# Optimization experiments

Measured on AMD Instinct MI355X. Metric: run time of the kernel, lower is better.

The kernel has to match this reference:

```python
import jax, jax.numpy as jnp
import numpy as np

B, T, F, D = 4, 512, 512, 256


def setup_inputs() -> dict:
    key = jax.random.key(0)
    ks = jax.random.split(key, 7)
    x = jax.random.normal(ks[0], (B, T, F), jnp.float32)
    state = jnp.zeros((B, D, D), jnp.float32)
    init = lambda k, shape, fan: jax.random.normal(k, shape, jnp.float32) / np.sqrt(fan).astype(np.float32)
    Wk = init(ks[1], (F, D), F)
    Wq = init(ks[2], (F, D), F)
    Wv = init(ks[3], (F, D), F)
    Wbeta = init(ks[4], (F, 1), F)
    gamma = jnp.ones((F,), jnp.float32)
    beta_ln = jnp.zeros((F,), jnp.float32)
    Wsc = init(ks[5], (F, D), F)
    bsc = jnp.zeros((D,), jnp.float32)
    return dict(x=x, state=state, Wk=Wk, Wq=Wq, Wv=Wv, Wbeta=Wbeta,
                gamma=gamma, beta_ln=beta_ln, Wsc=Wsc, bsc=bsc)


def _layernorm(x, gamma, beta):
    mu = x.mean(-1, keepdims=True)
    var = x.var(-1, keepdims=True)  # ddof=0, matches torch LayerNorm
    return (x - mu) * jax.lax.rsqrt(var + 1e-5) * gamma + beta


def reference(x, state, Wk, Wq, Wv, Wbeta, gamma, beta_ln, Wsc, bsc):
    xn = _layernorm(x, gamma, beta_ln)                       # [B,T,F]
    K = jax.nn.relu(xn @ Wk)                                 # [B,T,D]
    Q = jax.nn.relu(xn @ Wq)                                 # [B,T,D]
    V = xn @ Wv                                              # [B,T,D]
    beta = jax.nn.sigmoid(xn @ Wbeta)                        # [B,T,1]
    # sum normalization
    K = K / (1e-5 + K.sum(-1, keepdims=True))
    Q = Q / (1e-5 + Q.sum(-1, keepdims=True))

    def step(s, inp):
        k, v, b = inp                                        # k,v:[B,D], b:[B,1]
        vbar = jnp.einsum('bij,bj->bi', s, k)                # retrieve
        s = s + (b * (v - vbar))[:, :, None] * k[:, None, :] # outer-product write
        return s, s

    Kt = jnp.moveaxis(K, 1, 0)  # [T,B,D]
    Vt = jnp.moveaxis(V, 1, 0)
    bt = jnp.moveaxis(beta, 1, 0)  # [T,B,1]
    _, states = jax.lax.scan(step, state, (Kt, Vt, bt))      # [T,B,D,D]
    states = jnp.moveaxis(states, 0, 1)                      # [B,T,D,D]

    y = jnp.einsum('btij,btj->bti', states, Q)               # [B,T,D]
    y = y + xn @ Wsc + bsc                                   # residual shortcut
    return y, states
```

## Files before the change

kernel.cpp:

```cpp
#include <hip/hip_runtime.h>
#include <math.h>

#define Bc 4
#define Tc 512
#define Fc 512
#define Dc 256
#define RPB 8
#define PF 4
#define CH 16
#define RS 4
#define NC (Tc / CH)

typedef float floatx4 __attribute__((ext_vector_type(4)));

__device__ __forceinline__ float wred(float v) {
#pragma unroll
  for (int off = 32; off; off >>= 1) v += __shfl_xor(v, off, 64);
  return v;
}

__device__ __forceinline__ float rl(float v, int l) {
  return __int_as_float(__builtin_amdgcn_readlane(__float_as_int(v), l));
}

__device__ __forceinline__ void wred2_dpp(float& a, float& c) {
#define DPP_STEP(ctrl, rmask)                                                 \
  {                                                                           \
    float ta = __int_as_float(__builtin_amdgcn_update_dpp(                    \
        0, __float_as_int(a), (ctrl), (rmask), 0xf, true));                   \
    float tc = __int_as_float(__builtin_amdgcn_update_dpp(                    \
        0, __float_as_int(c), (ctrl), (rmask), 0xf, true));                   \
    a += ta;                                                                  \
    c += tc;                                                                  \
  }
  DPP_STEP(0x111, 0xf)
  DPP_STEP(0x112, 0xf)
  DPP_STEP(0x114, 0xf)
  DPP_STEP(0x118, 0xf)
  DPP_STEP(0x142, 0xa)
  DPP_STEP(0x143, 0xc)
#undef DPP_STEP
  a = rl(a, 63);
  c = rl(c, 63);
}

__global__ __launch_bounds__(256) void proj_kernel(
    const float* __restrict__ x, const float* __restrict__ Wk,
    const float* __restrict__ Wq, const float* __restrict__ Wv,
    const float* __restrict__ Wb, const float* __restrict__ gamma,
    const float* __restrict__ beta_ln, const float* __restrict__ Wsc,
    const float* __restrict__ bsc, float* __restrict__ Ko,
    float* __restrict__ Qo, float* __restrict__ Vo, float* __restrict__ ysco,
    float* __restrict__ betao, float* __restrict__ kqo) {
  __shared__ __align__(16) float xn[RPB][Fc];
  __shared__ float red[4][32];
  __shared__ float fin[32];

  const int tid = threadIdx.x;
  const int wave = tid >> 6, lane = tid & 63;
  const int row0 = blockIdx.x * RPB;

#pragma unroll
  for (int rr = 0; rr < 2; ++rr) {
    const int r = wave * 2 + rr;
    const float* xr = x + (size_t)(row0 + r) * Fc;
    float4 a = *(const float4*)&xr[lane * 8];
    float4 b = *(const float4*)&xr[lane * 8 + 4];
    float s8 = a.x + a.y + a.z + a.w + b.x + b.y + b.z + b.w;
    float mu = wred(s8) * (1.0f / Fc);
    float d0 = a.x - mu, d1 = a.y - mu, d2 = a.z - mu, d3 = a.w - mu;
    float d4 = b.x - mu, d5 = b.y - mu, d6 = b.z - mu, d7 = b.w - mu;
    float sq = d0 * d0 + d1 * d1 + d2 * d2 + d3 * d3 + d4 * d4 + d5 * d5 +
               d6 * d6 + d7 * d7;
    float var = wred(sq) * (1.0f / Fc);
    float rs = rsqrtf(var + 1e-5f);
    float4 g0 = *(const float4*)&gamma[lane * 8];
    float4 g1 = *(const float4*)&gamma[lane * 8 + 4];
    float4 bl0 = *(const float4*)&beta_ln[lane * 8];
    float4 bl1 = *(const float4*)&beta_ln[lane * 8 + 4];
    float4 o0 = make_float4(d0 * rs * g0.x + bl0.x, d1 * rs * g0.y + bl0.y,
                            d2 * rs * g0.z + bl0.z, d3 * rs * g0.w + bl0.w);
    float4 o1 = make_float4(d4 * rs * g1.x + bl1.x, d5 * rs * g1.y + bl1.y,
                            d6 * rs * g1.z + bl1.z, d7 * rs * g1.w + bl1.w);
    *(float4*)&xn[r][lane * 8] = o0;
    *(float4*)&xn[r][lane * 8 + 4] = o1;
  }
  __syncthreads();

  const int d = tid;
  float accK[RPB], accQ[RPB], accV[RPB], accS[RPB];
#pragma unroll
  for (int r = 0; r < RPB; ++r) accK[r] = accQ[r] = accV[r] = accS[r] = 0.0f;

  for (int f = 0; f < Fc; f += 4) {
    float wk[4], wq[4], wv[4], ws[4];
#pragma unroll
    for (int ff = 0; ff < 4; ++ff) {
      wk[ff] = Wk[(size_t)(f + ff) * Dc + d];
      wq[ff] = Wq[(size_t)(f + ff) * Dc + d];
      wv[ff] = Wv[(size_t)(f + ff) * Dc + d];
      ws[ff] = Wsc[(size_t)(f + ff) * Dc + d];
    }
#pragma unroll
    for (int r = 0; r < RPB; ++r) {
      float4 xr = *(const float4*)&xn[r][f];
      accK[r] = fmaf(xr.w, wk[3], fmaf(xr.z, wk[2], fmaf(xr.y, wk[1], fmaf(xr.x, wk[0], accK[r]))));
      accQ[r] = fmaf(xr.w, wq[3], fmaf(xr.z, wq[2], fmaf(xr.y, wq[1], fmaf(xr.x, wq[0], accQ[r]))));
      accV[r] = fmaf(xr.w, wv[3], fmaf(xr.z, wv[2], fmaf(xr.y, wv[1], fmaf(xr.x, wv[0], accV[r]))));
      accS[r] = fmaf(xr.w, ws[3], fmaf(xr.z, ws[2], fmaf(xr.y, ws[1], fmaf(xr.x, ws[0], accS[r]))));
    }
  }

  float pk[RPB], pq[RPB];
#pragma unroll
  for (int r = 0; r < RPB; ++r) {
    pk[r] = fmaxf(accK[r], 0.0f);
    pq[r] = fmaxf(accQ[r], 0.0f);
  }
#pragma unroll
  for (int r = 0; r < RPB; ++r) {
    float p0 = wred(pk[r]);
    float p1 = wred(pq[r]);
    float p2 = wred(pk[r] * pq[r]);
    float pb = xn[r][tid] * Wb[tid] + xn[r][tid + 256] * Wb[tid + 256];
    float p3 = wred(pb);
    if (lane == 0) {
      red[wave][r * 4 + 0] = p0;
      red[wave][r * 4 + 1] = p1;
      red[wave][r * 4 + 2] = p2;
      red[wave][r * 4 + 3] = p3;
    }
  }
  __syncthreads();
  if (tid < 32) fin[tid] = red[0][tid] + red[1][tid] + red[2][tid] + red[3][tid];
  __syncthreads();

#pragma unroll
  for (int r = 0; r < RPB; ++r) {
    size_t row = (size_t)(row0 + r);
    float invK = 1.0f / (1e-5f + fin[r * 4 + 0]);
    float invQ = 1.0f / (1e-5f + fin[r * 4 + 1]);
    Ko[row * Dc + d] = pk[r] * invK;
    Qo[row * Dc + d] = pq[r] * invQ;
    Vo[row * Dc + d] = accV[r];
    ysco[row * Dc + d] = accS[r] + bsc[d];
  }
  if (tid < RPB) {
    size_t row = (size_t)(row0 + tid);
    float invK = 1.0f / (1e-5f + fin[tid * 4 + 0]);
    float invQ = 1.0f / (1e-5f + fin[tid * 4 + 1]);
    betao[row] = 1.0f / (1.0f + expf(-fin[tid * 4 + 3]));
    kqo[row] = fin[tid * 4 + 2] * invK * invQ;
  }
}

__global__ __launch_bounds__(512) void scan_kernel(
    const float* __restrict__ S0, const float* __restrict__ K,
    const float* __restrict__ Q, const float* __restrict__ V,
    const float* __restrict__ ysc, const float* __restrict__ beta,
    const float* __restrict__ kq, float* __restrict__ yout,
    float* __restrict__ states) {
  __shared__ __align__(16) float ring_k[RS][CH][Dc];
  __shared__ float2 ring_uy[RS][CH][4];
  __shared__ int prog_a[4];
  __shared__ int prog_b[4];

  const int tid = threadIdx.x;
  const int wave = tid >> 6, lane = tid & 63;
  const int bid = blockIdx.x;
  const int xcd = bid & 7;
  const int slot = bid >> 3;
  const int b = xcd >> 1;
  const int sub = ((xcd & 1) << 5) | slot;
  const int i0 = sub * 4;

  if (tid < 4) {
    prog_a[tid] = 0;
    prog_b[tid] = 0;
  }
  __syncthreads();

  if (wave < 4) {
    const int i = i0 + wave;
    float4 s = *(const float4*)&S0[((size_t)(b * Dc + i)) * Dc + lane * 4];

    const float* Kb = K + (size_t)b * Tc * Dc;
    const float* Qb = Q + (size_t)b * Tc * Dc;
    const float* Vb = V + (size_t)b * Tc * Dc;
    const float* Yb = ysc + (size_t)b * Tc * Dc;
    const float* bb_p = beta + (size_t)b * Tc;
    const float* kq_p = kq + (size_t)b * Tc;

    float4 kb[PF], qb[PF];
#pragma unroll
    for (int j = 0; j < PF; ++j) {
      kb[j] = *(const float4*)&Kb[(size_t)j * Dc + lane * 4];
      qb[j] = *(const float4*)&Qb[(size_t)j * Dc + lane * 4];
    }
    const int sl = lane & 15;
    float vcur = Vb[(size_t)sl * Dc + i];
    float ycur = Yb[(size_t)sl * Dc + i];
    float bcur = bb_p[sl];
    float kqcur = kq_p[sl];

    for (int c = 0; c < NC; ++c) {
      if (c >= RS) {
        const int need = c - RS + 1;
#pragma unroll
        for (int m = 0; m < 4; ++m) {
          while (__hip_atomic_load(&prog_b[m], __ATOMIC_ACQUIRE,
                                   __HIP_MEMORY_SCOPE_WORKGROUP) < need)
            __builtin_amdgcn_s_sleep(2);
        }
      }
      const int cn = (c + 1 < NC) ? c + 1 : c;
      const int tbn = cn * CH;
      float vnxt = Vb[(size_t)(tbn + sl) * Dc + i];
      float ynxt = Yb[(size_t)(tbn + sl) * Dc + i];
      float bnxt = bb_p[tbn + sl];
      float kqnxt = kq_p[tbn + sl];

      const int r = c & (RS - 1);
      const int tb = c * CH;
#pragma unroll
      for (int j = 0; j < CH; ++j) {
        const int t = tb + j;
        const float4 k = kb[j & (PF - 1)];
        const float4 q = qb[j & (PF - 1)];
        const float vv = rl(vcur, j);
        const float yb = rl(ycur, j);
        const float bbs = rl(bcur, j);
        const float kqv = rl(kqcur, j);

        const int tn = (t + PF < Tc) ? t + PF : Tc - 1;
        kb[j & (PF - 1)] = *(const float4*)&Kb[(size_t)tn * Dc + lane * 4];
        qb[j & (PF - 1)] = *(const float4*)&Qb[(size_t)tn * Dc + lane * 4];

        float a = (s.x * k.x + s.y * k.y) + (s.z * k.z + s.w * k.w);
        float c2 = (s.x * q.x + s.y * q.y) + (s.z * q.z + s.w * q.w);
        wred2_dpp(a, c2);

        const float wcoef = bbs * (vv - a);
        s.x = fmaf(wcoef, k.x, s.x);
        s.y = fmaf(wcoef, k.y, s.y);
        s.z = fmaf(wcoef, k.z, s.z);
        s.w = fmaf(wcoef, k.w, s.w);

        if (wave == (j & 3)) *(float4*)&ring_k[r][j][lane * 4] = k;
        if (lane == 0) {
          float2 uy;
          uy.x = wcoef;
          uy.y = c2 + wcoef * kqv + yb;
          ring_uy[r][j][wave] = uy;
        }
      }
      __threadfence_block();
      __hip_atomic_store(&prog_a[wave], c + 1, __ATOMIC_RELEASE,
                         __HIP_MEMORY_SCOPE_WORKGROUP);
      vcur = vnxt;
      ycur = ynxt;
      bcur = bnxt;
      kqcur = kqnxt;
    }
  } else {
    const int wv = wave - 4;
    const int i = i0 + wv;
    float4 s = *(const float4*)&S0[((size_t)(b * Dc + i)) * Dc + lane * 4];

    for (int c = 0; c < NC; ++c) {
      const int need = c + 1;
#pragma unroll
      for (int m = 0; m < 4; ++m) {
        while (__hip_atomic_load(&prog_a[m], __ATOMIC_ACQUIRE,
                                 __HIP_MEMORY_SCOPE_WORKGROUP) < need)
          __builtin_amdgcn_s_sleep(2);
      }

      const int r = c & (RS - 1);
      const int tb = c * CH;
#pragma unroll
      for (int j = 0; j < CH; ++j) {
        const float2 uy = ring_uy[r][j][wv];
        const float4 k = *(const float4*)&ring_k[r][j][lane * 4];
        s.x = fmaf(uy.x, k.x, s.x);
        s.y = fmaf(uy.x, k.y, s.y);
        s.z = fmaf(uy.x, k.z, s.z);
        s.w = fmaf(uy.x, k.w, s.w);
        floatx4 sv;
        sv.x = s.x; sv.y = s.y; sv.z = s.z; sv.w = s.w;
        __builtin_nontemporal_store(
            sv, (floatx4*)&states[(((size_t)b * Tc + tb + j) * Dc + i) * Dc +
                                  lane * 4]);
        if (lane == 0) yout[((size_t)b * Tc + tb + j) * Dc + i] = uy.y;
      }
      __threadfence_block();
      __hip_atomic_store(&prog_b[wv], c + 1, __ATOMIC_RELEASE,
                         __HIP_MEMORY_SCOPE_WORKGROUP);
    }
  }
}

extern "C" void kernel_launch(void* const* d_in, const int* in_sizes, int n_in,
                              void* d_out, int out_size, void* d_ws,
                              size_t ws_size, hipStream_t stream) {
  const float* x = (const float*)d_in[0];
  const float* S0 = (const float*)d_in[1];
  const float* Wk = (const float*)d_in[2];
  const float* Wq = (const float*)d_in[3];
  const float* Wv = (const float*)d_in[4];
  const float* Wb = (const float*)d_in[5];
  const float* gamma = (const float*)d_in[6];
  const float* beta_ln = (const float*)d_in[7];
  const float* Wsc = (const float*)d_in[8];
  const float* bsc = (const float*)d_in[9];

  float* out = (float*)d_out;
  float* yout = out;
  float* states = out + (size_t)Bc * Tc * Dc;

  const size_t BTD = (size_t)Bc * Tc * Dc;
  float* ws = (float*)d_ws;
  float* K = ws;
  float* Q = K + BTD;
  float* V = Q + BTD;
  float* ysc = V + BTD;
  float* beta = ysc + BTD;
  float* kq = beta + (size_t)Bc * Tc;

  proj_kernel<<<(Bc * Tc) / RPB, 256, 0, stream>>>(
      x, Wk, Wq, Wv, Wb, gamma, beta_ln, Wsc, bsc, K, Q, V, ysc, beta, kq);
  scan_kernel<<<(Bc * Dc) / 4, 512, 0, stream>>>(S0, K, Q, V, ysc, beta, kq,
                                                 yout, states);
}
```

Baseline: 155.7 us.

## Split projection kernel into column-split GEMM pass and normalization pass

The fused projection kernel becomes two kernels. The first launches twice as many blocks, and each one computes half the output columns for 4 of the 8 rows per thread, which cuts per-thread accumulator registers and raises parallelism (launch_bounds set to 2 blocks per CU). The second kernel recomputes the layernorm, reloads the unnormalized K/Q from global memory, and does the row-sum reductions, beta and kq. This costs an extra kernel launch, a second layernorm pass, and an extra global round-trip of K and Q.

```diff
diff --git a/kernel.cpp b/kernel.cpp
--- a/kernel.cpp
+++ b/kernel.cpp
@@ -44,22 +44,11 @@
   c = rl(c, 63);
 }
 
-__global__ __launch_bounds__(256) void proj_kernel(
-    const float* __restrict__ x, const float* __restrict__ Wk,
-    const float* __restrict__ Wq, const float* __restrict__ Wv,
-    const float* __restrict__ Wb, const float* __restrict__ gamma,
-    const float* __restrict__ beta_ln, const float* __restrict__ Wsc,
-    const float* __restrict__ bsc, float* __restrict__ Ko,
-    float* __restrict__ Qo, float* __restrict__ Vo, float* __restrict__ ysco,
-    float* __restrict__ betao, float* __restrict__ kqo) {
-  __shared__ __align__(16) float xn[RPB][Fc];
-  __shared__ float red[4][32];
-  __shared__ float fin[32];
-
-  const int tid = threadIdx.x;
-  const int wave = tid >> 6, lane = tid & 63;
-  const int row0 = blockIdx.x * RPB;
-
+__device__ __forceinline__ void ln_rows(const float* __restrict__ x,
+                                        const float* __restrict__ gamma,
+                                        const float* __restrict__ beta_ln,
+                                        int row0, int wave, int lane,
+                                        float (*xnL)[Fc]) {
 #pragma unroll
   for (int rr = 0; rr < 2; ++rr) {
     const int r = wave * 2 + rr;
@@ -82,28 +71,47 @@
                             d2 * rs * g0.z + bl0.z, d3 * rs * g0.w + bl0.w);
     float4 o1 = make_float4(d4 * rs * g1.x + bl1.x, d5 * rs * g1.y + bl1.y,
                             d6 * rs * g1.z + bl1.z, d7 * rs * g1.w + bl1.w);
-    *(float4*)&xn[r][lane * 8] = o0;
-    *(float4*)&xn[r][lane * 8 + 4] = o1;
-  }
-  __syncthreads();
-
-  const int d = tid;
-  float accK[RPB], accQ[RPB], accV[RPB], accS[RPB];
-#pragma unroll
-  for (int r = 0; r < RPB; ++r) accK[r] = accQ[r] = accV[r] = accS[r] = 0.0f;
+    *(float4*)&xnL[r][lane * 8] = o0;
+    *(float4*)&xnL[r][lane * 8 + 4] = o1;
+  }
+}
+
+__global__ __launch_bounds__(256, 2) void proj1_kernel(
+    const float* __restrict__ x, const float* __restrict__ Wk,
+    const float* __restrict__ Wq, const float* __restrict__ Wv,
+    const float* __restrict__ gamma, const float* __restrict__ beta_ln,
+    const float* __restrict__ Wsc, const float* __restrict__ bsc,
+    float* __restrict__ Ko, float* __restrict__ Qo, float* __restrict__ Vo,
+    float* __restrict__ ysco) {
+  __shared__ __align__(16) float xn[RPB][Fc];
+
+  const int tid = threadIdx.x;
+  const int wave = tid >> 6, lane = tid & 63;
+  const int bid = blockIdx.x;
+  const int half = bid & 1;
+  const int row0 = (bid >> 1) * RPB;
+  const int col = half * 128 + (tid & 127);
+  const int rg = tid >> 7;
+
+  ln_rows(x, gamma, beta_ln, row0, wave, lane, xn);
+  __syncthreads();
+
+  float accK[4], accQ[4], accV[4], accS[4];
+#pragma unroll
+  for (int r = 0; r < 4; ++r) accK[r] = accQ[r] = accV[r] = accS[r] = 0.0f;
 
   for (int f = 0; f < Fc; f += 4) {
     float wk[4], wq[4], wv[4], ws[4];
 #pragma unroll
     for (int ff = 0; ff < 4; ++ff) {
-      wk[ff] = Wk[(size_t)(f + ff) * Dc + d];
-      wq[ff] = Wq[(size_t)(f + ff) * Dc + d];
-      wv[ff] = Wv[(size_t)(f + ff) * Dc + d];
-      ws[ff] = Wsc[(size_t)(f + ff) * Dc + d];
-    }
-#pragma unroll
-    for (int r = 0; r < RPB; ++r) {
-      float4 xr = *(const float4*)&xn[r][f];
+      wk[ff] = Wk[(size_t)(f + ff) * Dc + col];
+      wq[ff] = Wq[(size_t)(f + ff) * Dc + col];
+      wv[ff] = Wv[(size_t)(f + ff) * Dc + col];
+      ws[ff] = Wsc[(size_t)(f + ff) * Dc + col];
+    }
+#pragma unroll
+    for (int r = 0; r < 4; ++r) {
+      float4 xr = *(const float4*)&xn[rg * 4 + r][f];
       accK[r] = fmaf(xr.w, wk[3], fmaf(xr.z, wk[2], fmaf(xr.y, wk[1], fmaf(xr.x, wk[0], accK[r]))));
       accQ[r] = fmaf(xr.w, wq[3], fmaf(xr.z, wq[2], fmaf(xr.y, wq[1], fmaf(xr.x, wq[0], accQ[r]))));
       accV[r] = fmaf(xr.w, wv[3], fmaf(xr.z, wv[2], fmaf(xr.y, wv[1], fmaf(xr.x, wv[0], accV[r]))));
@@ -111,11 +119,39 @@
     }
   }
 
+  const float bs = bsc[col];
+#pragma unroll
+  for (int r = 0; r < 4; ++r) {
+    const size_t row = (size_t)(row0 + rg * 4 + r);
+    Ko[row * Dc + col] = fmaxf(accK[r], 0.0f);
+    Qo[row * Dc + col] = fmaxf(accQ[r], 0.0f);
+    Vo[row * Dc + col] = accV[r];
+    ysco[row * Dc + col] = accS[r] + bs;
+  }
+}
+
+__global__ __launch_bounds__(256) void proj2_kernel(
+    const float* __restrict__ x, const float* __restrict__ Wb,
+    const float* __restrict__ gamma, const float* __restrict__ beta_ln,
+    float* __restrict__ Ko, float* __restrict__ Qo, float* __restrict__ betao,
+    float* __restrict__ kqo) {
+  __shared__ __align__(16) float xn[RPB][Fc];
+  __shared__ float red[4][32];
+  __shared__ float fin[32];
+
+  const int tid = threadIdx.x;
+  const int wave = tid >> 6, lane = tid & 63;
+  const int row0 = blockIdx.x * RPB;
+
+  ln_rows(x, gamma, beta_ln, row0, wave, lane, xn);
+  __syncthreads();
+
+  const int d = tid;
   float pk[RPB], pq[RPB];
 #pragma unroll
   for (int r = 0; r < RPB; ++r) {
-    pk[r] = fmaxf(accK[r], 0.0f);
-    pq[r] = fmaxf(accQ[r], 0.0f);
+    pk[r] = Ko[(size_t)(row0 + r) * Dc + d];
+    pq[r] = Qo[(size_t)(row0 + r) * Dc + d];
   }
 #pragma unroll
   for (int r = 0; r < RPB; ++r) {
@@ -137,16 +173,14 @@
 
 #pragma unroll
   for (int r = 0; r < RPB; ++r) {
-    size_t row = (size_t)(row0 + r);
+    const size_t row = (size_t)(row0 + r);
     float invK = 1.0f / (1e-5f + fin[r * 4 + 0]);
     float invQ = 1.0f / (1e-5f + fin[r * 4 + 1]);
     Ko[row * Dc + d] = pk[r] * invK;
     Qo[row * Dc + d] = pq[r] * invQ;
-    Vo[row * Dc + d] = accV[r];
-    ysco[row * Dc + d] = accS[r] + bsc[d];
   }
   if (tid < RPB) {
-    size_t row = (size_t)(row0 + tid);
+    const size_t row = (size_t)(row0 + tid);
     float invK = 1.0f / (1e-5f + fin[tid * 4 + 0]);
     float invQ = 1.0f / (1e-5f + fin[tid * 4 + 1]);
     betao[row] = 1.0f / (1.0f + expf(-fin[tid * 4 + 3]));
@@ -327,8 +361,10 @@
   float* beta = ysc + BTD;
   float* kq = beta + (size_t)Bc * Tc;
 
-  proj_kernel<<<(Bc * Tc) / RPB, 256, 0, stream>>>(
-      x, Wk, Wq, Wv, Wb, gamma, beta_ln, Wsc, bsc, K, Q, V, ysc, beta, kq);
+  proj1_kernel<<<(Bc * Tc) / RPB * 2, 256, 0, stream>>>(
+      x, Wk, Wq, Wv, gamma, beta_ln, Wsc, bsc, K, Q, V, ysc);
+  proj2_kernel<<<(Bc * Tc) / RPB, 256, 0, stream>>>(x, Wb, gamma, beta_ln, K,
+                                                    Q, beta, kq);
   scan_kernel<<<(Bc * Dc) / 4, 512, 0, stream>>>(S0, K, Q, V, ysc, beta, kq,
                                                  yout, states);
 }
```

New measurement: 153.8 us. About the same (-1.2%).
